# Kernel tuning notes

Measured on AMD Instinct MI355X. Metric: run time of the kernel, lower is better.

The kernel has to match this reference:

```python
import jax, jax.numpy as jnp
import numpy as np

N_JOB, N_SKILL = 100000, 20000
H, D = 4, 64            # heads, per-head dim (hidden_channels)
F_DIM = H * D           # 256 = heads * hidden_channels
IN = 256                # in_channels
E_SJ, E_JJ, E_JS = 500000, 500000, 250000


def setup_inputs() -> dict:
    key = jax.random.key(0)
    ks = jax.random.split(key, 24)
    rn = lambda k, s, sc=0.05: jax.random.normal(k, s, dtype=jnp.float32) * sc
    z = lambda s: jnp.zeros(s, jnp.float32)
    return dict(
        x_job=rn(ks[0], (N_JOB, IN), 1.0),
        x_skill=rn(ks[1], (N_SKILL, IN), 1.0),
        W_job=rn(ks[2], (IN, F_DIM)), b_job=z((F_DIM,)),
        W_skill=rn(ks[3], (IN, F_DIM)), b_skill=z((F_DIM,)),
        a_src_sj=rn(ks[4], (H, D)), a_dst_sj=rn(ks[5], (H, D)),
        a_src_jj=rn(ks[6], (H, D)), a_dst_jj=rn(ks[7], (H, D)),
        a_src_js=rn(ks[8], (H, D)), a_dst_js=rn(ks[9], (H, D)),
        q=rn(ks[10], (F_DIM,)), Wk=rn(ks[11], (F_DIM, F_DIM)), bk=z((F_DIM,)),
        W1=rn(ks[12], (F_DIM, F_DIM)), b1=z((F_DIM,)),
        W2=rn(ks[13], (F_DIM, 1)), b2=z((1,)),
        ei_sj_src=jax.random.randint(ks[14], (E_SJ,), 0, N_SKILL),
        ei_sj_dst=jax.random.randint(ks[15], (E_SJ,), 0, N_JOB),
        ei_jj_src=jax.random.randint(ks[16], (E_JJ,), 0, N_JOB),
        ei_jj_dst=jax.random.randint(ks[17], (E_JJ,), 0, N_JOB),
        ei_js_src=jax.random.randint(ks[18], (E_JS,), 0, N_JOB),
        ei_js_dst=jax.random.randint(ks[19], (E_JS,), 0, N_SKILL),
    )


def _gat(x_src, x_dst, a_src, a_dst, src, dst, n_dst):
    # x_src: [Ns,H,D], x_dst: [Nd,H,D]; GAT-style node-level attention per edge type.
    al = jnp.einsum('nhd,hd->nh', x_src, a_src)[src] + jnp.einsum('nhd,hd->nh', x_dst, a_dst)[dst]
    al = jax.nn.leaky_relu(al, 0.2)                      # [E,H]
    amax = jax.lax.stop_gradient(jax.ops.segment_max(al, dst, n_dst))
    e = jnp.exp(al - amax[dst])
    denom = jax.ops.segment_sum(e, dst, n_dst)
    alpha = e / (denom[dst] + 1e-16)                     # softmax over incoming edges per dst
    out = jax.ops.segment_sum(x_src[src] * alpha[:, :, None], dst, n_dst)  # [Nd,H,D]
    return jax.nn.relu(out.reshape(n_dst, H * D))


def _group(outs, q, Wk, bk):
    # semantic-level attention across edge types (shared q, k_lin)
    stk = jnp.stack(outs)                                # [M,N,F]
    score = jnp.einsum('f,mf->m', q, jnp.tanh(stk @ Wk + bk).mean(1))
    attn = jax.nn.softmax(score)
    return jnp.einsum('m,mnf->nf', attn, stk)


def reference(x_job, x_skill, W_job, b_job, W_skill, b_skill,
              a_src_sj, a_dst_sj, a_src_jj, a_dst_jj, a_src_js, a_dst_js,
              q, Wk, bk, W1, b1, W2, b2,
              ei_sj_src, ei_sj_dst, ei_jj_src, ei_jj_dst, ei_js_src, ei_js_dst):
    h_job = (x_job @ W_job + b_job).reshape(N_JOB, H, D)
    h_skill = (x_skill @ W_skill + b_skill).reshape(N_SKILL, H, D)
    out_sj = _gat(h_skill, h_job, a_src_sj, a_dst_sj, ei_sj_src, ei_sj_dst, N_JOB)
    out_jj = _gat(h_job, h_job, a_src_jj, a_dst_jj, ei_jj_src, ei_jj_dst, N_JOB)
    out_js = _gat(h_job, h_skill, a_src_js, a_dst_js, ei_js_src, ei_js_dst, N_SKILL)
    job = _group([out_sj, out_jj], q, Wk, bk)            # 'job' node type
    _ = _group([out_js], q, Wk, bk)                      # 'skill' node type (unused by head)
    # dropout is identity in eval mode; MLP head (mlp_layers=2)
    h = jax.nn.relu(job @ W1 + b1)
    return (h @ W2 + b2)[:, 0]
```

## Files before the change

### kernel.cpp

```cpp
#include <hip/hip_runtime.h>
#include <hip/hip_bf16.h>
#include <math.h>

#define SCAN_B 256

typedef __attribute__((ext_vector_type(8))) short bf16x8;
typedef __attribute__((ext_vector_type(4))) float f32x4;

__device__ __forceinline__ unsigned short f2bf(float f) {
    __hip_bfloat16 h = __float2bfloat16(f);
    return *(unsigned short*)&h;
}
__device__ __forceinline__ float bf2f(unsigned short u) {
    unsigned v = ((unsigned)u) << 16;
    return __uint_as_float(v);
}
__device__ __forceinline__ float lrelu(float x) { return (x >= 0.f) ? x : 0.2f * x; }

__device__ __forceinline__ unsigned blend2(unsigned a, unsigned b, float c0, float c1) {
    float alo = bf2f((unsigned short)(a & 0xffff)), ahi = bf2f((unsigned short)(a >> 16));
    float blo = bf2f((unsigned short)(b & 0xffff)), bhi = bf2f((unsigned short)(b >> 16));
    unsigned short rlo = f2bf(c0 * alo + c1 * blo);
    unsigned short rhi = f2bf(c0 * ahi + c1 * bhi);
    return (unsigned)rlo | ((unsigned)rhi << 16);
}

template<int MODE, int NV, int AF32>
__launch_bounds__(512)
__global__ void gemm_mfma(const float* __restrict__ Af32,
                          const unsigned short* __restrict__ Abf,
                          const unsigned short* __restrict__ A2bf,
                          const unsigned short* __restrict__ Bt,
                          const float* __restrict__ bias,
                          const float* __restrict__ vq,
                          const float* __restrict__ b2p,
                          const float* __restrict__ attn2,
                          unsigned short* __restrict__ outh,
                          float* __restrict__ outf,
                          float* __restrict__ scoreSlot,
                          const float* __restrict__ av0,
                          const float* __restrict__ av1,
                          const float* __restrict__ av2,
                          float* __restrict__ lo0,
                          float* __restrict__ lo1,
                          float* __restrict__ lo2,
                          int M)
{
    __shared__ __align__(16) char sm[49152];
    __shared__ float red8[8];
    const int t    = threadIdx.x;
    const int lane = t & 63, wid = t >> 6;
    const int wr = wid >> 2, wc = wid & 3;
    const long row0 = (long)blockIdx.x * 128;
    const char* Ab = (const char*)((MODE == 1 && blockIdx.y == 1) ? A2bf : Abf);
    const char* A2 = (const char*)A2bf;
    const char* Bb = (const char*)Bt;

    float blend0 = 0.f, blend1 = 0.f;
    if (MODE == 2) { blend0 = attn2[0]; blend1 = attn2[1]; }

    f32x4 acc[4][4];
#pragma unroll
    for (int m = 0; m < 4; ++m)
#pragma unroll
        for (int n = 0; n < 4; ++n) acc[m][n] = (f32x4){0.f, 0.f, 0.f, 0.f};

    for (int k0 = 0; k0 < 256; k0 += 64) {
#pragma unroll
        for (int rep = 0; rep < 2; ++rep) {
            int idx = rep * 512 + t;
            int row = idx >> 3, colb = (idx & 7) << 4;
            uint4 v;
            if (AF32) {
                long grow = row0 + row;
                if (grow < M) {
                    const float* sp = Af32 + grow * 256 + k0 + ((idx & 7) << 3);
                    float4 f0 = *(const float4*)sp;
                    float4 f1 = *(const float4*)(sp + 4);
                    v.x = (unsigned)f2bf(f0.x) | ((unsigned)f2bf(f0.y) << 16);
                    v.y = (unsigned)f2bf(f0.z) | ((unsigned)f2bf(f0.w) << 16);
                    v.z = (unsigned)f2bf(f1.x) | ((unsigned)f2bf(f1.y) << 16);
                    v.w = (unsigned)f2bf(f1.z) | ((unsigned)f2bf(f1.w) << 16);
                } else {
                    v = make_uint4(0u, 0u, 0u, 0u);
                }
            } else {
                v = *(const uint4*)(Ab + (row0 + row) * 512 + k0 * 2 + colb);
                if (MODE == 2) {
                    uint4 v2 = *(const uint4*)(A2 + (row0 + row) * 512 + k0 * 2 + colb);
                    v.x = blend2(v.x, v2.x, blend0, blend1);
                    v.y = blend2(v.y, v2.y, blend0, blend1);
                    v.z = blend2(v.z, v2.z, blend0, blend1);
                    v.w = blend2(v.w, v2.w, blend0, blend1);
                }
            }
            *(uint4*)&sm[row * 128 + (colb ^ ((row & 7) << 4))] = v;
        }
#pragma unroll
        for (int rep = 0; rep < 4; ++rep) {
            int idx = rep * 512 + t;
            int n = idx >> 3, colb = (idx & 7) << 4;
            uint4 v = *(const uint4*)(Bb + n * 512 + k0 * 2 + colb);
            *(uint4*)&sm[16384 + n * 128 + (colb ^ ((n & 7) << 4))] = v;
        }
        __syncthreads();
#pragma unroll
        for (int kki = 0; kki < 2; ++kki) {
            const int kb = kki * 64 + ((lane >> 4) << 4);
            bf16x8 a[4], b[4];
#pragma unroll
            for (int m = 0; m < 4; ++m) {
                int row = wr * 64 + m * 16 + (lane & 15);
                a[m] = *(const bf16x8*)&sm[row * 128 + (kb ^ ((row & 7) << 4))];
            }
#pragma unroll
            for (int n = 0; n < 4; ++n) {
                int nr = wc * 64 + n * 16 + (lane & 15);
                b[n] = *(const bf16x8*)&sm[16384 + nr * 128 + (kb ^ ((nr & 7) << 4))];
            }
#pragma unroll
            for (int m = 0; m < 4; ++m)
#pragma unroll
                for (int n = 0; n < 4; ++n)
                    acc[m][n] = __builtin_amdgcn_mfma_f32_16x16x32_bf16(a[m], b[n], acc[m][n], 0, 0, 0);
        }
        __syncthreads();
    }

    const int colbase = wc * 64 + (lane & 15);
    const int rbase   = wr * 64 + ((lane >> 4) << 2);
    float bv[4];
#pragma unroll
    for (int n = 0; n < 4; ++n) bv[n] = bias[colbase + n * 16];

    if (MODE == 0) {
        float areg[(NV > 0) ? NV : 1][4];
#pragma unroll
        for (int v = 0; v < NV; ++v) {
            const float* av = (v == 0) ? av0 : (v == 1) ? av1 : av2;
#pragma unroll
            for (int n = 0; n < 4; ++n) areg[v][n] = av[colbase + n * 16];
        }
#pragma unroll
        for (int m = 0; m < 4; ++m) {
#pragma unroll
            for (int j = 0; j < 4; ++j) {
                long row = row0 + rbase + m * 16 + j;
                float hv[4];
#pragma unroll
                for (int n = 0; n < 4; ++n) hv[n] = acc[m][n][j] + bv[n];
                if (row < M) {
#pragma unroll
                    for (int n = 0; n < 4; ++n)
                        outh[row * 256 + colbase + n * 16] = f2bf(hv[n]);
                }
#pragma unroll
                for (int v = 0; v < NV; ++v) {
                    float p = hv[0] * areg[v][0] + hv[1] * areg[v][1]
                            + hv[2] * areg[v][2] + hv[3] * areg[v][3];
                    p += __shfl_xor(p, 1); p += __shfl_xor(p, 2);
                    p += __shfl_xor(p, 4); p += __shfl_xor(p, 8);
                    if ((lane & 15) == 0 && row < M) {
                        float* lo = (v == 0) ? lo0 : (v == 1) ? lo1 : lo2;
                        lo[row * 4 + wc] = p;
                    }
                }
            }
        }
    } else if (MODE == 1) {
        float p = 0.f;
        float qv[4];
#pragma unroll
        for (int n = 0; n < 4; ++n) qv[n] = vq[colbase + n * 16];
#pragma unroll
        for (int n = 0; n < 4; ++n) {
#pragma unroll
            for (int m = 0; m < 4; ++m) {
                long row = row0 + rbase + m * 16;
#pragma unroll
                for (int j = 0; j < 4; ++j)
                    if (row + j < M) p += qv[n] * tanhf(acc[m][n][j] + bv[n]);
            }
        }
#pragma unroll
        for (int off = 32; off > 0; off >>= 1) p += __shfl_xor(p, off);
        if (lane == 0) red8[wid] = p;
        __syncthreads();
        if (t == 0) {
            float s = 0.f;
#pragma unroll
            for (int i = 0; i < 8; ++i) s += red8[i];
            atomicAdd(&scoreSlot[blockIdx.y], s);
        }
    } else {
        float* redC = (float*)sm;
        float b2v = b2p[0];
        float wv[4];
#pragma unroll
        for (int n = 0; n < 4; ++n) wv[n] = vq[colbase + n * 16];
#pragma unroll
        for (int m = 0; m < 4; ++m) {
#pragma unroll
            for (int j = 0; j < 4; ++j) {
                float s = 0.f;
#pragma unroll
                for (int n = 0; n < 4; ++n)
                    s += fmaxf(acc[m][n][j] + bv[n], 0.f) * wv[n];
                s += __shfl_xor(s, 1); s += __shfl_xor(s, 2);
                s += __shfl_xor(s, 4); s += __shfl_xor(s, 8);
                if ((lane & 15) == 0) {
                    int lrow = wr * 64 + m * 16 + ((lane >> 4) << 2) + j;
                    redC[lrow * 4 + wc] = s;
                }
            }
        }
        __syncthreads();
        if (t < 128) {
            long row = row0 + t;
            if (row < M)
                outf[row] = redC[t * 4 + 0] + redC[t * 4 + 1]
                          + redC[t * 4 + 2] + redC[t * 4 + 3] + b2v;
        }
    }
}

__global__ void transpose_cast4(const float* __restrict__ W0, const float* __restrict__ W1s,
                                const float* __restrict__ W2s, const float* __restrict__ W3s,
                                unsigned short* __restrict__ T0, unsigned short* __restrict__ T1,
                                unsigned short* __restrict__ T2, unsigned short* __restrict__ T3)
{
    const float* W = (blockIdx.y == 0) ? W0 : (blockIdx.y == 1) ? W1s : (blockIdx.y == 2) ? W2s : W3s;
    unsigned short* T = (blockIdx.y == 0) ? T0 : (blockIdx.y == 1) ? T1 : (blockIdx.y == 2) ? T2 : T3;
    int n = blockIdx.x, k = threadIdx.x;
    T[n * 256 + k] = f2bf(W[k * 256 + n]);
}

__global__ void hist2(const int* __restrict__ d0, int E0, int* __restrict__ g0,
                      const int* __restrict__ d1, int E1, int* __restrict__ g1)
{
    int e = blockIdx.x * 256 + threadIdx.x;
    if (blockIdx.y == 0) { if (e < E0) atomicAdd(&g0[d0[e]], 1); }
    else                 { if (e < E1) atomicAdd(&g1[d1[e]], 1); }
}

__global__ void scan_bsum2(const int* __restrict__ g0, const int* __restrict__ g1, int n,
                           int* __restrict__ p0, int* __restrict__ p1)
{
    const int* deg = blockIdx.y ? g1 : g0;
    int* part      = blockIdx.y ? p1 : p0;
    __shared__ int smem[SCAN_B];
    int i = blockIdx.x * SCAN_B + threadIdx.x;
    smem[threadIdx.x] = (i < n) ? deg[i] : 0;
    __syncthreads();
    for (int off = SCAN_B / 2; off > 0; off >>= 1) {
        if (threadIdx.x < off) smem[threadIdx.x] += smem[threadIdx.x + off];
        __syncthreads();
    }
    if (threadIdx.x == 0) part[blockIdx.x] = smem[0];
}

__global__ void scan_part2(int* __restrict__ p0, int* __restrict__ p1, int nb)
{
    int* part = blockIdx.y ? p1 : p0;
    __shared__ int smem[1024];
    int t = threadIdx.x;
    int v = (t < nb) ? part[t] : 0;
    smem[t] = v;
    __syncthreads();
    for (int off = 1; off < 1024; off <<= 1) {
        int add = (t >= off) ? smem[t - off] : 0;
        __syncthreads();
        smem[t] += add;
        __syncthreads();
    }
    if (t < nb) part[t] = smem[t] - v;
}

__global__ void scan_final2(const int* __restrict__ g0, const int* __restrict__ g1, int n,
                            const int* __restrict__ p0, const int* __restrict__ p1,
                            int* __restrict__ r0, int* __restrict__ r1, int E0, int E1)
{
    const int* deg = blockIdx.y ? g1 : g0;
    const int* part = blockIdx.y ? p1 : p0;
    int* rowptr = blockIdx.y ? r1 : r0;
    int E = blockIdx.y ? E1 : E0;
    __shared__ int smem[SCAN_B];
    int t = threadIdx.x;
    int i = blockIdx.x * SCAN_B + t;
    int v = (i < n) ? deg[i] : 0;
    smem[t] = v;
    __syncthreads();
    for (int off = 1; off < SCAN_B; off <<= 1) {
        int add = (t >= off) ? smem[t - off] : 0;
        __syncthreads();
        smem[t] += add;
        __syncthreads();
    }
    if (i < n) rowptr[i] = part[blockIdx.x] + smem[t] - v;
    if (blockIdx.x == 0 && t == 0) rowptr[n] = E;
}

__global__ void fill_csr2(const int* __restrict__ d0, const int* __restrict__ s0arr, int E0,
                          const int* __restrict__ r0, int* __restrict__ c0, int* __restrict__ o0,
                          const int* __restrict__ d1, const int* __restrict__ s1arr, int E1,
                          const int* __restrict__ r1, int* __restrict__ c1, int* __restrict__ o1)
{
    int e = blockIdx.x * 256 + threadIdx.x;
    if (blockIdx.y == 0) {
        if (e < E0) { int d = d0[e]; int s = atomicAdd(&c0[d], 1); o0[r0[d] + s] = s0arr[e]; }
    } else {
        if (e < E1) { int d = d1[e]; int s = atomicAdd(&c1[d], 1); o1[r1[d] + s] = s1arr[e]; }
    }
}

__launch_bounds__(256)
__global__ void gat_fused(const unsigned short* __restrict__ xs0,
                          const unsigned short* __restrict__ xs1,
                          const float* __restrict__ als0, const float* __restrict__ als1,
                          const float* __restrict__ ald0, const float* __restrict__ ald1,
                          const int* __restrict__ rp0, const int* __restrict__ rp1,
                          const int* __restrict__ csr0, const int* __restrict__ csr1,
                          int N,
                          unsigned short* __restrict__ out0,
                          unsigned short* __restrict__ out1)
{
    const int et = blockIdx.y;
    const unsigned short* xsrc = et ? xs1 : xs0;
    const float* als = et ? als1 : als0;
    const float* ald = et ? ald1 : ald0;
    const int* rowptr = et ? rp1 : rp0;
    const int* csr    = et ? csr1 : csr0;
    unsigned short* outb = et ? out1 : out0;

    __shared__ __align__(16) float lw[4][4 * 64];
    __shared__ __align__(16) int   ls[4][64];
    const int wv   = threadIdx.x >> 6;
    const int w    = (int)((blockIdx.x * 256 + threadIdx.x) >> 6);
    const int lane = threadIdx.x & 63;
    if (w >= N) return;
    const int beg = rowptr[w], end = rowptr[w + 1];
    const int deg = end - beg;
    const int h = lane >> 4;
    const float4 d4 = *(const float4*)&ald[(size_t)w * 4];
    const unsigned loffb = (unsigned)(lane << 3);
    const char* xb = (const char*)xsrc;

    float accA[4] = {0.f, 0.f, 0.f, 0.f};
    float accB[4] = {0.f, 0.f, 0.f, 0.f};
    float dn = 0.f;

    if (deg <= 64) {
        if (lane < deg) {
            int es = csr[beg + lane];
            float4 a = *(const float4*)&als[(size_t)es * 4];
            ls[wv][lane] = es;
            lw[wv][0 * 64 + lane] = __expf(lrelu(a.x + d4.x));
            lw[wv][1 * 64 + lane] = __expf(lrelu(a.y + d4.y));
            lw[wv][2 * 64 + lane] = __expf(lrelu(a.z + d4.z));
            lw[wv][3 * 64 + lane] = __expf(lrelu(a.w + d4.w));
        }
        int i = 0;
        for (; i + 4 <= deg; i += 4) {
            int4   s4  = *(const int4*)&ls[wv][i];
            float4 wx4 = *(const float4*)&lw[wv][h * 64 + i];
            ushort4 x0 = *(const ushort4*)(xb + ((unsigned)s4.x * 512u + loffb));
            ushort4 x1 = *(const ushort4*)(xb + ((unsigned)s4.y * 512u + loffb));
            ushort4 x2 = *(const ushort4*)(xb + ((unsigned)s4.z * 512u + loffb));
            ushort4 x3 = *(const ushort4*)(xb + ((unsigned)s4.w * 512u + loffb));
            dn += wx4.x + wx4.y + wx4.z + wx4.w;
            accA[0] += wx4.x * bf2f(x0.x); accA[1] += wx4.x * bf2f(x0.y);
            accA[2] += wx4.x * bf2f(x0.z); accA[3] += wx4.x * bf2f(x0.w);
            accB[0] += wx4.y * bf2f(x1.x); accB[1] += wx4.y * bf2f(x1.y);
            accB[2] += wx4.y * bf2f(x1.z); accB[3] += wx4.y * bf2f(x1.w);
            accA[0] += wx4.z * bf2f(x2.x); accA[1] += wx4.z * bf2f(x2.y);
            accA[2] += wx4.z * bf2f(x2.z); accA[3] += wx4.z * bf2f(x2.w);
            accB[0] += wx4.w * bf2f(x3.x); accB[1] += wx4.w * bf2f(x3.y);
            accB[2] += wx4.w * bf2f(x3.z); accB[3] += wx4.w * bf2f(x3.w);
        }
        for (; i < deg; ++i) {
            int s = ls[wv][i];
            float wx = lw[wv][h * 64 + i];
            ushort4 xu = *(const ushort4*)(xb + ((unsigned)s * 512u + loffb));
            dn += wx;
            accA[0] += wx * bf2f(xu.x); accA[1] += wx * bf2f(xu.y);
            accA[2] += wx * bf2f(xu.z); accA[3] += wx * bf2f(xu.w);
        }
    } else {
        for (int c = beg; c < end; c += 64) {
            int cnt = min(64, end - c);
            if (lane < cnt) {
                int es = csr[c + lane];
                float4 a = *(const float4*)&als[(size_t)es * 4];
                ls[wv][lane] = es;
                lw[wv][0 * 64 + lane] = __expf(lrelu(a.x + d4.x));
                lw[wv][1 * 64 + lane] = __expf(lrelu(a.y + d4.y));
                lw[wv][2 * 64 + lane] = __expf(lrelu(a.z + d4.z));
                lw[wv][3 * 64 + lane] = __expf(lrelu(a.w + d4.w));
            }
            int i = 0;
            for (; i + 4 <= cnt; i += 4) {
                int4   s4  = *(const int4*)&ls[wv][i];
                float4 wx4 = *(const float4*)&lw[wv][h * 64 + i];
                ushort4 x0 = *(const ushort4*)(xb + ((unsigned)s4.x * 512u + loffb));
                ushort4 x1 = *(const ushort4*)(xb + ((unsigned)s4.y * 512u + loffb));
                ushort4 x2 = *(const ushort4*)(xb + ((unsigned)s4.z * 512u + loffb));
                ushort4 x3 = *(const ushort4*)(xb + ((unsigned)s4.w * 512u + loffb));
                dn += wx4.x + wx4.y + wx4.z + wx4.w;
                accA[0] += wx4.x * bf2f(x0.x); accA[1] += wx4.x * bf2f(x0.y);
                accA[2] += wx4.x * bf2f(x0.z); accA[3] += wx4.x * bf2f(x0.w);
                accB[0] += wx4.y * bf2f(x1.x); accB[1] += wx4.y * bf2f(x1.y);
                accB[2] += wx4.y * bf2f(x1.z); accB[3] += wx4.y * bf2f(x1.w);
                accA[0] += wx4.z * bf2f(x2.x); accA[1] += wx4.z * bf2f(x2.y);
                accA[2] += wx4.z * bf2f(x2.z); accA[3] += wx4.z * bf2f(x2.w);
                accB[0] += wx4.w * bf2f(x3.x); accB[1] += wx4.w * bf2f(x3.y);
                accB[2] += wx4.w * bf2f(x3.z); accB[3] += wx4.w * bf2f(x3.w);
            }
            for (; i < cnt; ++i) {
                int s = ls[wv][i];
                float wx = lw[wv][h * 64 + i];
                ushort4 xu = *(const ushort4*)(xb + ((unsigned)s * 512u + loffb));
                dn += wx;
                accA[0] += wx * bf2f(xu.x); accA[1] += wx * bf2f(xu.y);
                accA[2] += wx * bf2f(xu.z); accA[3] += wx * bf2f(xu.w);
            }
        }
    }

#pragma unroll
    for (int j = 0; j < 4; ++j) accA[j] += accB[j];
    float inv = 1.f / (dn + 1e-16f);
    ushort4 uo;
    uo.x = f2bf(fmaxf(accA[0] * inv, 0.f));
    uo.y = f2bf(fmaxf(accA[1] * inv, 0.f));
    uo.z = f2bf(fmaxf(accA[2] * inv, 0.f));
    uo.w = f2bf(fmaxf(accA[3] * inv, 0.f));
    *(ushort4*)&outb[(size_t)w * 256 + (lane << 2)] = uo;
}

__global__ void attn_k(const float* __restrict__ score, float* __restrict__ attn, float invN)
{
    if (threadIdx.x == 0 && blockIdx.x == 0) {
        float s0 = score[0] * invN, s1 = score[1] * invN;
        float m  = fmaxf(s0, s1);
        float e0 = expf(s0 - m), e1 = expf(s1 - m);
        float dsum = e0 + e1;
        attn[0] = e0 / dsum;
        attn[1] = e1 / dsum;
    }
}

extern "C" void kernel_launch(void* const* d_in, const int* in_sizes, int n_in,
                              void* d_out, int out_size, void* d_ws, size_t ws_size,
                              hipStream_t stream)
{
    const float* x_job    = (const float*)d_in[0];
    const float* x_skill  = (const float*)d_in[1];
    const float* W_job    = (const float*)d_in[2];
    const float* b_job    = (const float*)d_in[3];
    const float* W_skill  = (const float*)d_in[4];
    const float* b_skill  = (const float*)d_in[5];
    const float* a_src_sj = (const float*)d_in[6];
    const float* a_dst_sj = (const float*)d_in[7];
    const float* a_src_jj = (const float*)d_in[8];
    const float* a_dst_jj = (const float*)d_in[9];
    const float* q_vec = (const float*)d_in[12];
    const float* Wk    = (const float*)d_in[13];
    const float* bk    = (const float*)d_in[14];
    const float* W1    = (const float*)d_in[15];
    const float* b1    = (const float*)d_in[16];
    const float* W2    = (const float*)d_in[17];
    const float* b2    = (const float*)d_in[18];
    const int* ei_sj_src = (const int*)d_in[19];
    const int* ei_sj_dst = (const int*)d_in[20];
    const int* ei_jj_src = (const int*)d_in[21];
    const int* ei_jj_dst = (const int*)d_in[22];

    const int NJ   = in_sizes[0] / 256;
    const int NS   = in_sizes[1] / 256;
    const int E_sj = in_sizes[19];
    const int E_jj = in_sizes[21];
    const int Emax = (E_sj > E_jj) ? E_sj : E_jj;
    const int gmJ  = (NJ + 127) / 128, gmS = (NS + 127) / 128;
    const long MpadJ = (long)gmJ * 128, MpadS = (long)gmS * 128;

    char* ws   = (char*)d_ws;
    size_t off = 0;
    auto alloc = [&](size_t bytes) { void* p = ws + off; off += (bytes + 255) & ~(size_t)255; return p; };
    unsigned short* h_job_bf   = (unsigned short*)alloc(MpadJ * 256 * 2);
    unsigned short* h_skill_bf = (unsigned short*)alloc(MpadS * 256 * 2);
    unsigned short* Wjob_t  = (unsigned short*)alloc(256 * 256 * 2);
    unsigned short* Wskl_t  = (unsigned short*)alloc(256 * 256 * 2);
    unsigned short* Wk_t    = (unsigned short*)alloc(256 * 256 * 2);
    unsigned short* W1_t    = (unsigned short*)alloc(256 * 256 * 2);
    unsigned short* out_sj_bf = (unsigned short*)alloc(MpadJ * 256 * 2);
    unsigned short* out_jj_bf = (unsigned short*)alloc(MpadJ * 256 * 2);
    float* ald_sj  = (float*)alloc((size_t)NJ * 4 * 4);
    float* als_jj  = (float*)alloc((size_t)NJ * 4 * 4);
    float* ald_jj  = (float*)alloc((size_t)NJ * 4 * 4);
    float* als_sj  = (float*)alloc((size_t)NS * 4 * 4);
    float* score  = (float*)alloc(64 * 4);
    float* attn   = score + 2;
    size_t zoff0 = off;
    int* deg_sj = (int*)alloc((size_t)NJ * 4);
    int* deg_jj = (int*)alloc((size_t)NJ * 4);
    int* rp_sj  = (int*)alloc(((size_t)NJ + 1) * 4);
    int* rp_jj  = (int*)alloc(((size_t)NJ + 1) * 4);
    int* part_a = (int*)alloc(1024 * 4);
    int* part_b = (int*)alloc(1024 * 4);
    int* cur_sj = (int*)alloc((size_t)NJ * 4);
    int* cur_jj = (int*)alloc((size_t)NJ * 4);
    size_t zoff1 = off;
    int* csr_sj = (int*)alloc((size_t)E_sj * 4);
    int* csr_jj = (int*)alloc((size_t)E_jj * 4);
    (void)ws_size; (void)n_in;

    hipMemsetAsync(score, 0, 2 * 4, stream);
    hipMemsetAsync(ws + zoff0, 0, zoff1 - zoff0, stream);

    dim3 blk(256);
    int nbJ = (NJ + SCAN_B - 1) / SCAN_B;

    transpose_cast4<<<dim3(256, 4), blk, 0, stream>>>(
        W_job, W_skill, Wk, W1, Wjob_t, Wskl_t, Wk_t, W1_t);

    hist2<<<dim3((Emax + 255) / 256, 2), blk, 0, stream>>>(
        ei_sj_dst, E_sj, deg_sj, ei_jj_dst, E_jj, deg_jj);
    scan_bsum2<<<dim3(nbJ, 2), dim3(SCAN_B), 0, stream>>>(deg_sj, deg_jj, NJ, part_a, part_b);
    scan_part2<<<dim3(1, 2), dim3(1024), 0, stream>>>(part_a, part_b, nbJ);
    scan_final2<<<dim3(nbJ, 2), dim3(SCAN_B), 0, stream>>>(
        deg_sj, deg_jj, NJ, part_a, part_b, rp_sj, rp_jj, E_sj, E_jj);
    fill_csr2<<<dim3((Emax + 255) / 256, 2), blk, 0, stream>>>(
        ei_sj_dst, ei_sj_src, E_sj, rp_sj, cur_sj, csr_sj,
        ei_jj_dst, ei_jj_src, E_jj, rp_jj, cur_jj, csr_jj);

    gemm_mfma<0, 3, 1><<<dim3(gmJ), dim3(512), 0, stream>>>(
        x_job, nullptr, nullptr, Wjob_t, b_job, nullptr, nullptr, nullptr,
        h_job_bf, nullptr, nullptr,
        a_dst_sj, a_src_jj, a_dst_jj, ald_sj, als_jj, ald_jj, NJ);
    gemm_mfma<0, 1, 1><<<dim3(gmS), dim3(512), 0, stream>>>(
        x_skill, nullptr, nullptr, Wskl_t, b_skill, nullptr, nullptr, nullptr,
        h_skill_bf, nullptr, nullptr,
        a_src_sj, nullptr, nullptr, als_sj, nullptr, nullptr, NS);

    gat_fused<<<dim3((NJ + 3) / 4, 2), blk, 0, stream>>>(
        h_skill_bf, h_job_bf, als_sj, als_jj, ald_sj, ald_jj,
        rp_sj, rp_jj, csr_sj, csr_jj, NJ,
        out_sj_bf, out_jj_bf);

    gemm_mfma<1, 0, 0><<<dim3(gmJ, 2), dim3(512), 0, stream>>>(
        nullptr, out_sj_bf, out_jj_bf, Wk_t, bk, q_vec, nullptr, nullptr,
        nullptr, nullptr, score,
        nullptr, nullptr, nullptr, nullptr, nullptr, nullptr, NJ);
    attn_k<<<1, 64, 0, stream>>>(score, attn, 1.0f / (float)NJ);

    gemm_mfma<2, 0, 0><<<dim3(gmJ), dim3(512), 0, stream>>>(
        nullptr, out_sj_bf, out_jj_bf, W1_t, b1, W2, b2, attn,
        nullptr, (float*)d_out, nullptr,
        nullptr, nullptr, nullptr, nullptr, nullptr, nullptr, NJ);
}
```

Baseline: 394.6 us.

## Double-buffer GEMM K-loop with register prefetch of next A tile

```diff
diff --git a/kernel.cpp b/kernel.cpp
--- a/kernel.cpp
+++ b/kernel.cpp
@@ -26,7 +26,7 @@
 }
 
 template<int MODE, int NV, int AF32>
-__launch_bounds__(512)
+__launch_bounds__(512, 6)
 __global__ void gemm_mfma(const float* __restrict__ Af32,
                           const unsigned short* __restrict__ Abf,
                           const unsigned short* __restrict__ A2bf,
@@ -59,72 +59,88 @@
     float blend0 = 0.f, blend1 = 0.f;
     if (MODE == 2) { blend0 = attn2[0]; blend1 = attn2[1]; }
 
+    const int ar = t >> 2, aslot = t & 3;
+    const long agrow = row0 + ar;
+    const unsigned swA  = ((unsigned)(aslot << 4)) ^ ((unsigned)(((ar  >> 1) & 3) << 4));
+    const int bn0 = t >> 2, bn1 = 128 + (t >> 2);
+    const unsigned swB  = ((unsigned)(aslot << 4)) ^ ((unsigned)(((bn0 >> 1) & 3) << 4));
+
     f32x4 acc[4][4];
 #pragma unroll
     for (int m = 0; m < 4; ++m)
 #pragma unroll
         for (int n = 0; n < 4; ++n) acc[m][n] = (f32x4){0.f, 0.f, 0.f, 0.f};
 
-    for (int k0 = 0; k0 < 256; k0 += 64) {
-#pragma unroll
-        for (int rep = 0; rep < 2; ++rep) {
-            int idx = rep * 512 + t;
-            int row = idx >> 3, colb = (idx & 7) << 4;
-            uint4 v;
-            if (AF32) {
-                long grow = row0 + row;
-                if (grow < M) {
-                    const float* sp = Af32 + grow * 256 + k0 + ((idx & 7) << 3);
-                    float4 f0 = *(const float4*)sp;
-                    float4 f1 = *(const float4*)(sp + 4);
-                    v.x = (unsigned)f2bf(f0.x) | ((unsigned)f2bf(f0.y) << 16);
-                    v.y = (unsigned)f2bf(f0.z) | ((unsigned)f2bf(f0.w) << 16);
-                    v.z = (unsigned)f2bf(f1.x) | ((unsigned)f2bf(f1.y) << 16);
-                    v.w = (unsigned)f2bf(f1.z) | ((unsigned)f2bf(f1.w) << 16);
-                } else {
-                    v = make_uint4(0u, 0u, 0u, 0u);
-                }
-            } else {
-                v = *(const uint4*)(Ab + (row0 + row) * 512 + k0 * 2 + colb);
-                if (MODE == 2) {
-                    uint4 v2 = *(const uint4*)(A2 + (row0 + row) * 512 + k0 * 2 + colb);
-                    v.x = blend2(v.x, v2.x, blend0, blend1);
-                    v.y = blend2(v.y, v2.y, blend0, blend1);
-                    v.z = blend2(v.z, v2.z, blend0, blend1);
-                    v.w = blend2(v.w, v2.w, blend0, blend1);
-                }
-            }
-            *(uint4*)&sm[row * 128 + (colb ^ ((row & 7) << 4))] = v;
-        }
-#pragma unroll
-        for (int rep = 0; rep < 4; ++rep) {
-            int idx = rep * 512 + t;
-            int n = idx >> 3, colb = (idx & 7) << 4;
-            uint4 v = *(const uint4*)(Bb + n * 512 + k0 * 2 + colb);
-            *(uint4*)&sm[16384 + n * 128 + (colb ^ ((n & 7) << 4))] = v;
-        }
-        __syncthreads();
-#pragma unroll
-        for (int kki = 0; kki < 2; ++kki) {
-            const int kb = kki * 64 + ((lane >> 4) << 4);
-            bf16x8 a[4], b[4];
-#pragma unroll
-            for (int m = 0; m < 4; ++m) {
-                int row = wr * 64 + m * 16 + (lane & 15);
-                a[m] = *(const bf16x8*)&sm[row * 128 + (kb ^ ((row & 7) << 4))];
-            }
-#pragma unroll
-            for (int n = 0; n < 4; ++n) {
-                int nr = wc * 64 + n * 16 + (lane & 15);
-                b[n] = *(const bf16x8*)&sm[16384 + nr * 128 + (kb ^ ((nr & 7) << 4))];
-            }
-#pragma unroll
-            for (int m = 0; m < 4; ++m)
-#pragma unroll
-                for (int n = 0; n < 4; ++n)
-                    acc[m][n] = __builtin_amdgcn_mfma_f32_16x16x32_bf16(a[m], b[n], acc[m][n], 0, 0, 0);
-        }
-        __syncthreads();
+    float4 rF0, rF1;
+    uint4  rA, rA2;
+
+    auto loadA = [&](int k0) {
+        if (AF32) {
+            rF0 = make_float4(0.f, 0.f, 0.f, 0.f); rF1 = rF0;
+            if (agrow < M) {
+                const float* sp = Af32 + agrow * 256 + k0 + aslot * 8;
+                rF0 = *(const float4*)sp;
+                rF1 = *(const float4*)(sp + 4);
+            }
+        } else {
+            rA = *(const uint4*)(Ab + agrow * 512 + (long)k0 * 2 + aslot * 16);
+            if (MODE == 2)
+                rA2 = *(const uint4*)(A2 + agrow * 512 + (long)k0 * 2 + aslot * 16);
+        }
+    };
+    auto stage = [&](char* buf, int k0) {
+        uint4 v;
+        if (AF32) {
+            v.x = (unsigned)f2bf(rF0.x) | ((unsigned)f2bf(rF0.y) << 16);
+            v.y = (unsigned)f2bf(rF0.z) | ((unsigned)f2bf(rF0.w) << 16);
+            v.z = (unsigned)f2bf(rF1.x) | ((unsigned)f2bf(rF1.y) << 16);
+            v.w = (unsigned)f2bf(rF1.z) | ((unsigned)f2bf(rF1.w) << 16);
+        } else if (MODE == 2) {
+            v.x = blend2(rA.x, rA2.x, blend0, blend1);
+            v.y = blend2(rA.y, rA2.y, blend0, blend1);
+            v.z = blend2(rA.z, rA2.z, blend0, blend1);
+            v.w = blend2(rA.w, rA2.w, blend0, blend1);
+        } else {
+            v = rA;
+        }
+        *(uint4*)(buf + ar * 64 + swA) = v;
+        uint4 b0 = *(const uint4*)(Bb + (long)bn0 * 512 + (long)k0 * 2 + aslot * 16);
+        uint4 b1 = *(const uint4*)(Bb + (long)bn1 * 512 + (long)k0 * 2 + aslot * 16);
+        *(uint4*)(buf + 8192 + bn0 * 64 + swB) = b0;
+        *(uint4*)(buf + 8192 + bn1 * 64 + swB) = b1;
+    };
+    auto compute = [&](const char* buf) {
+        const int kb = (lane >> 4) << 4;
+        bf16x8 a[4], b[4];
+#pragma unroll
+        for (int m = 0; m < 4; ++m) {
+            int row = wr * 64 + m * 16 + (lane & 15);
+            a[m] = *(const bf16x8*)(buf + row * 64 + (kb ^ (((row >> 1) & 3) << 4)));
+        }
+#pragma unroll
+        for (int n = 0; n < 4; ++n) {
+            int nr = wc * 64 + n * 16 + (lane & 15);
+            b[n] = *(const bf16x8*)(buf + 8192 + nr * 64 + (kb ^ (((nr >> 1) & 3) << 4)));
+        }
+#pragma unroll
+        for (int m = 0; m < 4; ++m)
+#pragma unroll
+            for (int n = 0; n < 4; ++n)
+                acc[m][n] = __builtin_amdgcn_mfma_f32_16x16x32_bf16(a[m], b[n], acc[m][n], 0, 0, 0);
+    };
+
+    loadA(0);
+    stage(sm, 0);
+    __syncthreads();
+#pragma unroll
+    for (int kt = 0; kt < 8; ++kt) {
+        if (kt < 7) loadA((kt + 1) * 32);
+        compute(sm + (kt & 1) * 24576);
+        __syncthreads();
+        if (kt < 7) {
+            stage(sm + ((kt + 1) & 1) * 24576, (kt + 1) * 32);
+            __syncthreads();
+        }
     }
 
     const int colbase = wc * 64 + (lane & 15);
```

Result: slower. 846.9 us (+114.6%).

## Split projection and score GEMMs into 128x128 tiles with 256-thread blocks

Applied to the files above, without the earlier changes.

```diff
diff --git a/kernel.cpp b/kernel.cpp
--- a/kernel.cpp
+++ b/kernel.cpp
@@ -26,39 +26,35 @@
 }
 
 template<int MODE, int NV, int AF32>
-__launch_bounds__(512)
-__global__ void gemm_mfma(const float* __restrict__ Af32,
-                          const unsigned short* __restrict__ Abf,
-                          const unsigned short* __restrict__ A2bf,
-                          const unsigned short* __restrict__ Bt,
-                          const float* __restrict__ bias,
-                          const float* __restrict__ vq,
-                          const float* __restrict__ b2p,
-                          const float* __restrict__ attn2,
-                          unsigned short* __restrict__ outh,
-                          float* __restrict__ outf,
-                          float* __restrict__ scoreSlot,
-                          const float* __restrict__ av0,
-                          const float* __restrict__ av1,
-                          const float* __restrict__ av2,
-                          float* __restrict__ lo0,
-                          float* __restrict__ lo1,
-                          float* __restrict__ lo2,
-                          int M)
-{
-    __shared__ __align__(16) char sm[49152];
-    __shared__ float red8[8];
+__launch_bounds__(256)
+__global__ void gemm128(const float* __restrict__ Af32,
+                        const unsigned short* __restrict__ Abf,
+                        const unsigned short* __restrict__ A2bf,
+                        const unsigned short* __restrict__ Bt,
+                        const float* __restrict__ bias,
+                        const float* __restrict__ vq,
+                        unsigned short* __restrict__ outh,
+                        float* __restrict__ scoreSlot,
+                        const float* __restrict__ av0,
+                        const float* __restrict__ av1,
+                        const float* __restrict__ av2,
+                        float* __restrict__ lo0,
+                        float* __restrict__ lo1,
+                        float* __restrict__ lo2,
+                        int M)
+{
+    __shared__ __align__(16) char sm[32768];
+    __shared__ float red4[4];
     const int t    = threadIdx.x;
     const int lane = t & 63, wid = t >> 6;
-    const int wr = wid >> 2, wc = wid & 3;
+    const int wr = wid >> 1, wc = wid & 1;
+    const int ntile = (MODE == 1) ? (blockIdx.y & 1) : blockIdx.y;
+    const int atype = (MODE == 1) ? (blockIdx.y >> 1) : 0;
+    const int ncol0 = ntile * 128;
     const long row0 = (long)blockIdx.x * 128;
-    const char* Ab = (const char*)((MODE == 1 && blockIdx.y == 1) ? A2bf : Abf);
-    const char* A2 = (const char*)A2bf;
+    const char* Ab = (const char*)((MODE == 1 && atype == 1) ? A2bf : Abf);
     const char* Bb = (const char*)Bt;
 
-    float blend0 = 0.f, blend1 = 0.f;
-    if (MODE == 2) { blend0 = attn2[0]; blend1 = attn2[1]; }
-
     f32x4 acc[4][4];
 #pragma unroll
     for (int m = 0; m < 4; ++m)
@@ -67,8 +63,8 @@
 
     for (int k0 = 0; k0 < 256; k0 += 64) {
 #pragma unroll
-        for (int rep = 0; rep < 2; ++rep) {
-            int idx = rep * 512 + t;
+        for (int rep = 0; rep < 4; ++rep) {
+            int idx = rep * 256 + t;
             int row = idx >> 3, colb = (idx & 7) << 4;
             uint4 v;
             if (AF32) {
@@ -86,21 +82,14 @@
                 }
             } else {
                 v = *(const uint4*)(Ab + (row0 + row) * 512 + k0 * 2 + colb);
-                if (MODE == 2) {
-                    uint4 v2 = *(const uint4*)(A2 + (row0 + row) * 512 + k0 * 2 + colb);
-                    v.x = blend2(v.x, v2.x, blend0, blend1);
-                    v.y = blend2(v.y, v2.y, blend0, blend1);
-                    v.z = blend2(v.z, v2.z, blend0, blend1);
-                    v.w = blend2(v.w, v2.w, blend0, blend1);
-                }
             }
             *(uint4*)&sm[row * 128 + (colb ^ ((row & 7) << 4))] = v;
         }
 #pragma unroll
         for (int rep = 0; rep < 4; ++rep) {
-            int idx = rep * 512 + t;
+            int idx = rep * 256 + t;
             int n = idx >> 3, colb = (idx & 7) << 4;
-            uint4 v = *(const uint4*)(Bb + n * 512 + k0 * 2 + colb);
+            uint4 v = *(const uint4*)(Bb + (long)(ncol0 + n) * 512 + k0 * 2 + colb);
             *(uint4*)&sm[16384 + n * 128 + (colb ^ ((n & 7) << 4))] = v;
         }
         __syncthreads();
@@ -127,11 +116,11 @@
         __syncthreads();
     }
 
-    const int colbase = wc * 64 + (lane & 15);
-    const int rbase   = wr * 64 + ((lane >> 4) << 2);
+    const int colloc = wc * 64 + (lane & 15);
+    const int rbase  = wr * 64 + ((lane >> 4) << 2);
     float bv[4];
 #pragma unroll
-    for (int n = 0; n < 4; ++n) bv[n] = bias[colbase + n * 16];
+    for (int n = 0; n < 4; ++n) bv[n] = bias[ncol0 + colloc + n * 16];
 
     if (MODE == 0) {
         float areg[(NV > 0) ? NV : 1][4];
@@ -139,8 +128,9 @@
         for (int v = 0; v < NV; ++v) {
             const float* av = (v == 0) ? av0 : (v == 1) ? av1 : av2;
 #pragma unroll
-            for (int n = 0; n < 4; ++n) areg[v][n] = av[colbase + n * 16];
-        }
+            for (int n = 0; n < 4; ++n) areg[v][n] = av[ncol0 + colloc + n * 16];
+        }
+        const int headbase = ntile * 2 + wc;
 #pragma unroll
         for (int m = 0; m < 4; ++m) {
 #pragma unroll
@@ -152,7 +142,7 @@
                 if (row < M) {
 #pragma unroll
                     for (int n = 0; n < 4; ++n)
-                        outh[row * 256 + colbase + n * 16] = f2bf(hv[n]);
+                        outh[row * 256 + ncol0 + colloc + n * 16] = f2bf(hv[n]);
                 }
 #pragma unroll
                 for (int v = 0; v < NV; ++v) {
@@ -162,16 +152,16 @@
                     p += __shfl_xor(p, 4); p += __shfl_xor(p, 8);
                     if ((lane & 15) == 0 && row < M) {
                         float* lo = (v == 0) ? lo0 : (v == 1) ? lo1 : lo2;
-                        lo[row * 4 + wc] = p;
+                        lo[row * 4 + headbase] = p;
                     }
                 }
             }
         }
-    } else if (MODE == 1) {
+    } else {
         float p = 0.f;
         float qv[4];
 #pragma unroll
-        for (int n = 0; n < 4; ++n) qv[n] = vq[colbase + n * 16];
+        for (int n = 0; n < 4; ++n) qv[n] = vq[ncol0 + colloc + n * 16];
 #pragma unroll
         for (int n = 0; n < 4; ++n) {
 #pragma unroll
@@ -184,15 +174,99 @@
         }
 #pragma unroll
         for (int off = 32; off > 0; off >>= 1) p += __shfl_xor(p, off);
-        if (lane == 0) red8[wid] = p;
+        if (lane == 0) red4[wid] = p;
         __syncthreads();
         if (t == 0) {
-            float s = 0.f;
-#pragma unroll
-            for (int i = 0; i < 8; ++i) s += red8[i];
-            atomicAdd(&scoreSlot[blockIdx.y], s);
-        }
-    } else {
+            atomicAdd(&scoreSlot[atype], red4[0] + red4[1] + red4[2] + red4[3]);
+        }
+    }
+}
+
+template<int MODE, int NV, int AF32>
+__launch_bounds__(512)
+__global__ void gemm_mfma(const float* __restrict__ Af32,
+                          const unsigned short* __restrict__ Abf,
+                          const unsigned short* __restrict__ A2bf,
+                          const unsigned short* __restrict__ Bt,
+                          const float* __restrict__ bias,
+                          const float* __restrict__ vq,
+                          const float* __restrict__ b2p,
+                          const float* __restrict__ attn2,
+                          unsigned short* __restrict__ outh,
+                          float* __restrict__ outf,
+                          float* __restrict__ scoreSlot,
+                          int M)
+{
+    __shared__ __align__(16) char sm[49152];
+    const int t    = threadIdx.x;
+    const int lane = t & 63, wid = t >> 6;
+    const int wr = wid >> 2, wc = wid & 3;
+    const long row0 = (long)blockIdx.x * 128;
+    const char* Ab = (const char*)Abf;
+    const char* A2 = (const char*)A2bf;
+    const char* Bb = (const char*)Bt;
+
+    float blend0 = 0.f, blend1 = 0.f;
+    if (MODE == 2) { blend0 = attn2[0]; blend1 = attn2[1]; }
+
+    f32x4 acc[4][4];
+#pragma unroll
+    for (int m = 0; m < 4; ++m)
+#pragma unroll
+        for (int n = 0; n < 4; ++n) acc[m][n] = (f32x4){0.f, 0.f, 0.f, 0.f};
+
+    for (int k0 = 0; k0 < 256; k0 += 64) {
+#pragma unroll
+        for (int rep = 0; rep < 2; ++rep) {
+            int idx = rep * 512 + t;
+            int row = idx >> 3, colb = (idx & 7) << 4;
+            uint4 v = *(const uint4*)(Ab + (row0 + row) * 512 + k0 * 2 + colb);
+            if (MODE == 2) {
+                uint4 v2 = *(const uint4*)(A2 + (row0 + row) * 512 + k0 * 2 + colb);
+                v.x = blend2(v.x, v2.x, blend0, blend1);
+                v.y = blend2(v.y, v2.y, blend0, blend1);
+                v.z = blend2(v.z, v2.z, blend0, blend1);
+                v.w = blend2(v.w, v2.w, blend0, blend1);
+            }
+            *(uint4*)&sm[row * 128 + (colb ^ ((row & 7) << 4))] = v;
+        }
+#pragma unroll
+        for (int rep = 0; rep < 4; ++rep) {
+            int idx = rep * 512 + t;
+            int n = idx >> 3, colb = (idx & 7) << 4;
+            uint4 v = *(const uint4*)(Bb + n * 512 + k0 * 2 + colb);
+            *(uint4*)&sm[16384 + n * 128 + (colb ^ ((n & 7) << 4))] = v;
+        }
+        __syncthreads();
+#pragma unroll
+        for (int kki = 0; kki < 2; ++kki) {
+            const int kb = kki * 64 + ((lane >> 4) << 4);
+            bf16x8 a[4], b[4];
+#pragma unroll
+            for (int m = 0; m < 4; ++m) {
+                int row = wr * 64 + m * 16 + (lane & 15);
+                a[m] = *(const bf16x8*)&sm[row * 128 + (kb ^ ((row & 7) << 4))];
+            }
+#pragma unroll
+            for (int n = 0; n < 4; ++n) {
+                int nr = wc * 64 + n * 16 + (lane & 15);
+                b[n] = *(const bf16x8*)&sm[16384 + nr * 128 + (kb ^ ((nr & 7) << 4))];
+            }
+#pragma unroll
+            for (int m = 0; m < 4; ++m)
+#pragma unroll
+                for (int n = 0; n < 4; ++n)
+                    acc[m][n] = __builtin_amdgcn_mfma_f32_16x16x32_bf16(a[m], b[n], acc[m][n], 0, 0, 0);
+        }
+        __syncthreads();
+    }
+
+    const int colbase = wc * 64 + (lane & 15);
+    float bv[4];
+#pragma unroll
+    for (int n = 0; n < 4; ++n) bv[n] = bias[colbase + n * 16];
+
+    {
         float* redC = (float*)sm;
         float b2v = b2p[0];
         float wv[4];
@@ -313,6 +387,7 @@
     }
 }
 
+#define LWS 68
 __launch_bounds__(256)
 __global__ void gat_fused(const unsigned short* __restrict__ xs0,
                           const unsigned short* __restrict__ xs1,
@@ -332,7 +407,7 @@
     const int* csr    = et ? csr1 : csr0;
     unsigned short* outb = et ? out1 : out0;
 
-    __shared__ __align__(16) float lw[4][4 * 64];
+    __shared__ __align__(16) float lw[4][4 * LWS];
     __shared__ __align__(16) int   ls[4][64];
     const int wv   = threadIdx.x >> 6;
     const int w    = (int)((blockIdx.x * 256 + threadIdx.x) >> 6);
@@ -354,15 +429,15 @@
             int es = csr[beg + lane];
             float4 a = *(const float4*)&als[(size_t)es * 4];
             ls[wv][lane] = es;
-            lw[wv][0 * 64 + lane] = __expf(lrelu(a.x + d4.x));
-            lw[wv][1 * 64 + lane] = __expf(lrelu(a.y + d4.y));
-            lw[wv][2 * 64 + lane] = __expf(lrelu(a.z + d4.z));
-            lw[wv][3 * 64 + lane] = __expf(lrelu(a.w + d4.w));
+            lw[wv][0 * LWS + lane] = __expf(lrelu(a.x + d4.x));
+            lw[wv][1 * LWS + lane] = __expf(lrelu(a.y + d4.y));
+            lw[wv][2 * LWS + lane] = __expf(lrelu(a.z + d4.z));
+            lw[wv][3 * LWS + lane] = __expf(lrelu(a.w + d4.w));
         }
         int i = 0;
         for (; i + 4 <= deg; i += 4) {
             int4   s4  = *(const int4*)&ls[wv][i];
-            float4 wx4 = *(const float4*)&lw[wv][h * 64 + i];
+            float4 wx4 = *(const float4*)&lw[wv][h * LWS + i];
             ushort4 x0 = *(const ushort4*)(xb + ((unsigned)s4.x * 512u + loffb));
             ushort4 x1 = *(const ushort4*)(xb + ((unsigned)s4.y * 512u + loffb));
             ushort4 x2 = *(const ushort4*)(xb + ((unsigned)s4.z * 512u + loffb));
@@ -379,7 +454,7 @@
         }
         for (; i < deg; ++i) {
             int s = ls[wv][i];
-            float wx = lw[wv][h * 64 + i];
+            float wx = lw[wv][h * LWS + i];
             ushort4 xu = *(const ushort4*)(xb + ((unsigned)s * 512u + loffb));
             dn += wx;
             accA[0] += wx * bf2f(xu.x); accA[1] += wx * bf2f(xu.y);
@@ -392,15 +467,15 @@
                 int es = csr[c + lane];
                 float4 a = *(const float4*)&als[(size_t)es * 4];
                 ls[wv][lane] = es;
-                lw[wv][0 * 64 + lane] = __expf(lrelu(a.x + d4.x));
-                lw[wv][1 * 64 + lane] = __expf(lrelu(a.y + d4.y));
-                lw[wv][2 * 64 + lane] = __expf(lrelu(a.z + d4.z));
-                lw[wv][3 * 64 + lane] = __expf(lrelu(a.w + d4.w));
+                lw[wv][0 * LWS + lane] = __expf(lrelu(a.x + d4.x));
+                lw[wv][1 * LWS + lane] = __expf(lrelu(a.y + d4.y));
+                lw[wv][2 * LWS + lane] = __expf(lrelu(a.z + d4.z));
+                lw[wv][3 * LWS + lane] = __expf(lrelu(a.w + d4.w));
             }
             int i = 0;
             for (; i + 4 <= cnt; i += 4) {
                 int4   s4  = *(const int4*)&ls[wv][i];
-                float4 wx4 = *(const float4*)&lw[wv][h * 64 + i];
+                float4 wx4 = *(const float4*)&lw[wv][h * LWS + i];
                 ushort4 x0 = *(const ushort4*)(xb + ((unsigned)s4.x * 512u + loffb));
                 ushort4 x1 = *(const ushort4*)(xb + ((unsigned)s4.y * 512u + loffb));
                 ushort4 x2 = *(const ushort4*)(xb + ((unsigned)s4.z * 512u + loffb));
@@ -417,7 +492,7 @@
             }
             for (; i < cnt; ++i) {
                 int s = ls[wv][i];
-                float wx = lw[wv][h * 64 + i];
+                float wx = lw[wv][h * LWS + i];
                 ushort4 xu = *(const ushort4*)(xb + ((unsigned)s * 512u + loffb));
                 dn += wx;
                 accA[0] += wx * bf2f(xu.x); accA[1] += wx * bf2f(xu.y);
@@ -533,13 +608,13 @@
         ei_sj_dst, ei_sj_src, E_sj, rp_sj, cur_sj, csr_sj,
         ei_jj_dst, ei_jj_src, E_jj, rp_jj, cur_jj, csr_jj);
 
-    gemm_mfma<0, 3, 1><<<dim3(gmJ), dim3(512), 0, stream>>>(
-        x_job, nullptr, nullptr, Wjob_t, b_job, nullptr, nullptr, nullptr,
-        h_job_bf, nullptr, nullptr,
+    gemm128<0, 3, 1><<<dim3(gmJ, 2), dim3(256), 0, stream>>>(
+        x_job, nullptr, nullptr, Wjob_t, b_job, nullptr,
+        h_job_bf, nullptr,
         a_dst_sj, a_src_jj, a_dst_jj, ald_sj, als_jj, ald_jj, NJ);
-    gemm_mfma<0, 1, 1><<<dim3(gmS), dim3(512), 0, stream>>>(
-        x_skill, nullptr, nullptr, Wskl_t, b_skill, nullptr, nullptr, nullptr,
-        h_skill_bf, nullptr, nullptr,
+    gemm128<0, 1, 1><<<dim3(gmS, 2), dim3(256), 0, stream>>>(
+        x_skill, nullptr, nullptr, Wskl_t, b_skill, nullptr,
+        h_skill_bf, nullptr,
         a_src_sj, nullptr, nullptr, als_sj, nullptr, nullptr, NS);
 
     gat_fused<<<dim3((NJ + 3) / 4, 2), blk, 0, stream>>>(
@@ -547,14 +622,13 @@
         rp_sj, rp_jj, csr_sj, csr_jj, NJ,
         out_sj_bf, out_jj_bf);
 
-    gemm_mfma<1, 0, 0><<<dim3(gmJ, 2), dim3(512), 0, stream>>>(
-        nullptr, out_sj_bf, out_jj_bf, Wk_t, bk, q_vec, nullptr, nullptr,
-        nullptr, nullptr, score,
+    gemm128<1, 0, 0><<<dim3(gmJ, 4), dim3(256), 0, stream>>>(
+        nullptr, out_sj_bf, out_jj_bf, Wk_t, bk, q_vec,
+        nullptr, score,
         nullptr, nullptr, nullptr, nullptr, nullptr, nullptr, NJ);
     attn_k<<<1, 64, 0, stream>>>(score, attn, 1.0f / (float)NJ);
 
     gemm_mfma<2, 0, 0><<<dim3(gmJ), dim3(512), 0, stream>>>(
         nullptr, out_sj_bf, out_jj_bf, W1_t, b1, W2, b2, attn,
-        nullptr, (float*)d_out, nullptr,
-        nullptr, nullptr, nullptr, nullptr, nullptr, nullptr, NJ);
-}
+        nullptr, (float*)d_out, nullptr, NJ);
+}
```

Result: slower. 422.6 us (+7.1%).
